# Optimization experiments

Measured on AMD Instinct MI355X. Metric: run time of the kernel, lower is better.

The kernel has to match this reference:

```python
import jax, jax.numpy as jnp
import numpy as np

MARGIN = 0.5
HIERARCHY_LEVEL = 0
EPS = 1e-05


def setup_inputs() -> dict:
    key = jax.random.key(0)
    k1, k2, k3, k4 = jax.random.split(key, 4)
    n, m, d, L, n_classes = 4096, 32768, 128, 2, 100
    embeddings = jax.random.normal(k1, (n, d), dtype=jnp.float32)
    ref_embeddings = jax.random.normal(k2, (m, d), dtype=jnp.float32)
    labels = jax.random.randint(k3, (n, L), 0, n_classes, dtype=jnp.int64)
    ref_labels = jax.random.randint(k4, (m, L), 0, n_classes, dtype=jnp.int64)
    return {"embeddings": embeddings, "labels": labels,
            "ref_embeddings": ref_embeddings, "ref_labels": ref_labels}


def reference(embeddings, labels, ref_embeddings, ref_labels):
    # select hierarchy level
    lab = labels[:, HIERARCHY_LEVEL]          # [n]
    ref_lab = ref_labels[:, HIERARCHY_LEVEL]  # [m]
    n = embeddings.shape[0]
    sim = embeddings @ ref_embeddings.T       # [n, m]
    same = lab[:, None] == ref_lab[None, :]   # [n, m] bool
    # positive pairs: same label and sim < 1 - eps -> contribute (1 - sim)
    pos_mask = same & (sim < 1.0 - EPS)
    # negative pairs: different label and sim > margin -> contribute sim
    neg_mask = (~same) & (sim > MARGIN)
    pos_loss = jnp.sum(jnp.where(pos_mask, 1.0 - sim, 0.0))
    neg_loss = jnp.sum(jnp.where(neg_mask, sim, 0.0))
    return (pos_loss + neg_loss) / n
```

## Files before the change

kernel.cpp:

```cpp
#include <hip/hip_runtime.h>
#include <stdint.h>

#define N_EMB 4096
#define M_REF 32768
#define D_K   128
#define NCLS  100
#define BM    128
#define BN    64
#define NT_PER 16
#define COLCHUNK (BN * NT_PER)
#define NCCHUNK (M_REF / COLCHUNK)
#define NROWT  (N_EMB / BM)
#define XBLOCKS (NROWT * NCCHUNK)
#define RCAP 192
#define CCAP 768

typedef __attribute__((ext_vector_type(8))) short short8;
typedef __attribute__((ext_vector_type(4))) float float4v;

static __device__ __forceinline__ unsigned short f2bf(float f) {
    unsigned int u = __builtin_bit_cast(unsigned int, f);
    u += 0x7FFFu + ((u >> 16) & 1u);
    return (unsigned short)(u >> 16);
}

#define CVT_THREADS (768 * 256)

__global__ void cvt_kernel(const float* __restrict__ emb, const float* __restrict__ ref,
                           unsigned short* __restrict__ aw, unsigned short* __restrict__ bw,
                           float* __restrict__ out) {
    const int NA4 = N_EMB * D_K / 4;
    int i0 = blockIdx.x * 256 + threadIdx.x;
    if (i0 == 0) *out = 0.0f;
    #pragma unroll
    for (int k = 0; k < 6; ++k) {
        int i = i0 + k * CVT_THREADS;
        const float4* src;
        unsigned short* dst;
        int j;
        if (i < NA4) { src = (const float4*)emb; dst = aw; j = i; }
        else         { src = (const float4*)ref; dst = bw; j = i - NA4; }
        float4 v = src[j];
        ushort4 o;
        o.x = f2bf(v.x); o.y = f2bf(v.y); o.z = f2bf(v.z); o.w = f2bf(v.w);
        *(ushort4*)(dst + (size_t)j * 4) = o;
    }
}

static __device__ __forceinline__ void gld_lds16(const void* g, void* l) {
    __builtin_amdgcn_global_load_lds((__attribute__((address_space(1))) void*)g,
                                     (__attribute__((address_space(3))) void*)l,
                                     16, 0, 0);
}

template<int NI>
static __device__ __forceinline__ void stage_rows(const unsigned short* __restrict__ g,
                                                  unsigned short* l, int tid) {
    const int rlow = tid >> 4;
    const int sc   = (tid & 15) ^ rlow;
    const char* g0 = (const char*)g + (rlow * D_K + sc * 8) * 2;
    char* l0 = (char*)l + tid * 16;
    #pragma unroll
    for (int i = 0; i < NI; ++i)
        gld_lds16(g0 + (size_t)i * (16 * D_K * 2), l0 + i * 4096);
}

static __device__ __forceinline__ void stage_gather(const unsigned short* __restrict__ base,
                                                    const int* idxlist, int count,
                                                    unsigned short* l, int tid) {
    const int rlow = tid >> 4;
    const int sc   = (tid & 15) ^ rlow;
    char* l0 = (char*)l + tid * 16;
    #pragma unroll
    for (int i = 0; i < 4; ++i) {
        int r = i * 16 + rlow;
        if (r < count) {
            int gi = idxlist[r];
            gld_lds16((const char*)base + ((size_t)gi * D_K + sc * 8) * 2, l0 + i * 4096);
        }
    }
}

__launch_bounds__(256, 4)
__global__ void xbm_kernel(const unsigned short* __restrict__ aw,
                           const unsigned short* __restrict__ bw,
                           const int* __restrict__ lab,
                           const int* __restrict__ rlab,
                           float* __restrict__ out) {
    __shared__ unsigned short b_sm[2][BN * D_K];
    __shared__ float red_sm[4];
    __shared__ int rlist[RCAP], clist[CCAP];
    __shared__ int rcnt_s, ccnt_s;

    const int tid  = threadIdx.x;
    const int lane = tid & 63;
    const int wave = tid >> 6;
    const int quad = lane >> 4;
    const int l15  = lane & 15;

    float bsum = 0.0f;

    if (blockIdx.x >= NCLS) {
        const int gid = blockIdx.x - NCLS;
        const int rtile  = gid >> 5;
        const int cchunk = gid & 31;
        const int row0 = rtile * BM;
        const int col0 = cchunk * COLCHUNK;

        stage_rows<8>(aw + (size_t)row0 * D_K, &b_sm[0][0], tid);
        __syncthreads();

        short8 a_reg[2][4];
        #pragma unroll
        for (int mt = 0; mt < 2; ++mt) {
            int ml = wave * 32 + mt * 16 + l15;
            #pragma unroll
            for (int ks = 0; ks < 4; ++ks) {
                int cs = (ks * 4 + quad) ^ l15;
                a_reg[mt][ks] = *(const short8*)(&b_sm[0][0] + (size_t)ml * D_K + cs * 8);
            }
        }
        __syncthreads();

        stage_rows<4>(bw + (size_t)col0 * D_K, b_sm[0], tid);

        float lsum[4] = {0.0f, 0.0f, 0.0f, 0.0f};

        #define COMPUTE_TILE(BP)                                                  \
            {                                                                     \
                const unsigned short* bp_ = (BP);                                 \
                float4v acc[2][4] = {};                                           \
                _Pragma("unroll")                                                 \
                for (int ks = 0; ks < 4; ++ks) {                                  \
                    short8 breg[4];                                               \
                    _Pragma("unroll")                                             \
                    for (int nt = 0; nt < 4; ++nt) {                              \
                        int nl = nt * 16 + l15;                                   \
                        int cs = (ks * 4 + quad) ^ l15;                           \
                        breg[nt] = *(const short8*)(bp_ + (size_t)nl * D_K + cs * 8); \
                    }                                                             \
                    _Pragma("unroll")                                             \
                    for (int mt = 0; mt < 2; ++mt)                                \
                        _Pragma("unroll")                                         \
                        for (int nt = 0; nt < 4; ++nt)                            \
                            acc[mt][nt] = __builtin_amdgcn_mfma_f32_16x16x32_bf16(\
                                a_reg[mt][ks], breg[nt], acc[mt][nt], 0, 0, 0);   \
                }                                                                 \
                _Pragma("unroll")                                                 \
                for (int mt = 0; mt < 2; ++mt)                                    \
                    _Pragma("unroll")                                             \
                    for (int nt = 0; nt < 4; ++nt)                                \
                        _Pragma("unroll")                                         \
                        for (int r = 0; r < 4; ++r) {                             \
                            float s = acc[mt][nt][r];                             \
                            lsum[r] += (s > 0.5f) ? s : 0.0f;                     \
                        }                                                         \
            }

        #pragma unroll 1
        for (int t = 0; t < NT_PER; t += 2) {
            __syncthreads();
            stage_rows<4>(bw + (size_t)(col0 + (t + 1) * BN) * D_K, b_sm[1], tid);
            COMPUTE_TILE(b_sm[0]);
            __syncthreads();
            if (t + 2 < NT_PER)
                stage_rows<4>(bw + (size_t)(col0 + (t + 2) * BN) * D_K, b_sm[0], tid);
            COMPUTE_TILE(b_sm[1]);
        }
        bsum = (lsum[0] + lsum[1]) + (lsum[2] + lsum[3]);
    } else {
        const int cls = blockIdx.x;

        if (tid == 0) { rcnt_s = 0; ccnt_s = 0; }
        __syncthreads();
        for (int i = tid; i < N_EMB; i += 256)
            if (lab[i * 2] == cls) {
                int p = atomicAdd(&rcnt_s, 1);
                if (p < RCAP) rlist[p] = i;
            }
        for (int j = tid; j < M_REF; j += 256)
            if (rlab[j * 2] == cls) {
                int p = atomicAdd(&ccnt_s, 1);
                if (p < CCAP) clist[p] = j;
            }
        __syncthreads();
        const int rn = min(rcnt_s, RCAP), cn = min(ccnt_s, CCAP);

        for (int r0 = 0; r0 < rn; r0 += 64) {
            const int rch = min(64, rn - r0);
            __syncthreads();
            stage_gather(aw, rlist + r0, rch, b_sm[0], tid);
            for (int c0 = 0; c0 < cn; c0 += 64) {
                const int cch = min(64, cn - c0);
                __syncthreads();
                stage_gather(bw, clist + c0, cch, b_sm[1], tid);
                __syncthreads();
                const int slot = wave * 16 + l15;
                const bool cvalid = slot < cch;
                #pragma unroll 1
                for (int mt = 0; mt < 4; ++mt) {
                    if (mt * 16 >= rch) break;
                    float4v acc = {0.0f, 0.0f, 0.0f, 0.0f};
                    #pragma unroll
                    for (int ks = 0; ks < 4; ++ks) {
                        int cs = (ks * 4 + quad) ^ l15;
                        short8 a = *(const short8*)(b_sm[0] + (size_t)(mt * 16 + l15) * D_K + cs * 8);
                        short8 b = *(const short8*)(b_sm[1] + (size_t)slot * D_K + cs * 8);
                        acc = __builtin_amdgcn_mfma_f32_16x16x32_bf16(a, b, acc, 0, 0, 0);
                    }
                    #pragma unroll
                    for (int r = 0; r < 4; ++r) {
                        int m_loc = mt * 16 + quad * 4 + r;
                        if (cvalid && m_loc < rch) {
                            float s = acc[r];
                            bsum += fmaxf(1.0f - s, 0.0f) - ((s > 0.5f) ? s : 0.0f);
                        }
                    }
                }
            }
        }
    }

    #pragma unroll
    for (int off = 32; off > 0; off >>= 1)
        bsum += __shfl_down(bsum, off, 64);
    if (lane == 0) red_sm[wave] = bsum;
    __syncthreads();
    if (tid == 0) {
        float v = (red_sm[0] + red_sm[1] + red_sm[2] + red_sm[3]) * (1.0f / (float)N_EMB);
        atomicAdd(out, v);
    }
}

extern "C" void kernel_launch(void* const* d_in, const int* in_sizes, int n_in,
                              void* d_out, int out_size, void* d_ws, size_t ws_size,
                              hipStream_t stream) {
    const float* emb     = (const float*)d_in[0];
    const int*   labels  = (const int*)d_in[1];
    const float* ref     = (const float*)d_in[2];
    const int*   rlabels = (const int*)d_in[3];
    float* out = (float*)d_out;

    unsigned short* aw = (unsigned short*)d_ws;
    unsigned short* bw = aw + (size_t)N_EMB * D_K;

    cvt_kernel<<<768, 256, 0, stream>>>(emb, ref, aw, bw, out);
    xbm_kernel<<<XBLOCKS + NCLS, 256, 0, stream>>>(aw, bw, labels, rlabels, out);
}
```

Baseline: 127.0 us.

## Widen GEMM tile to 128x128 and build class lists in the convert kernel

```diff
diff --git a/kernel.cpp b/kernel.cpp
--- a/kernel.cpp
+++ b/kernel.cpp
@@ -6,7 +6,7 @@
 #define D_K   128
 #define NCLS  100
 #define BM    128
-#define BN    64
+#define BN    128
 #define NT_PER 16
 #define COLCHUNK (BN * NT_PER)
 #define NCCHUNK (M_REF / COLCHUNK)
@@ -28,22 +28,41 @@
 
 __global__ void cvt_kernel(const float* __restrict__ emb, const float* __restrict__ ref,
                            unsigned short* __restrict__ aw, unsigned short* __restrict__ bw,
+                           const int* __restrict__ lab, const int* __restrict__ rlab,
+                           int* __restrict__ cnt_row, int* __restrict__ cnt_col,
+                           int* __restrict__ rowlist, int* __restrict__ collist,
                            float* __restrict__ out) {
-    const int NA4 = N_EMB * D_K / 4;
-    int i0 = blockIdx.x * 256 + threadIdx.x;
-    if (i0 == 0) *out = 0.0f;
-    #pragma unroll
-    for (int k = 0; k < 6; ++k) {
-        int i = i0 + k * CVT_THREADS;
-        const float4* src;
-        unsigned short* dst;
-        int j;
-        if (i < NA4) { src = (const float4*)emb; dst = aw; j = i; }
-        else         { src = (const float4*)ref; dst = bw; j = i - NA4; }
-        float4 v = src[j];
-        ushort4 o;
-        o.x = f2bf(v.x); o.y = f2bf(v.y); o.z = f2bf(v.z); o.w = f2bf(v.w);
-        *(ushort4*)(dst + (size_t)j * 4) = o;
+    if (blockIdx.x < 768) {
+        const int NA4 = N_EMB * D_K / 4;
+        int i0 = blockIdx.x * 256 + threadIdx.x;
+        if (i0 == 0) *out = 0.0f;
+        #pragma unroll
+        for (int k = 0; k < 6; ++k) {
+            int i = i0 + k * CVT_THREADS;
+            const float4* src;
+            unsigned short* dst;
+            int j;
+            if (i < NA4) { src = (const float4*)emb; dst = aw; j = i; }
+            else         { src = (const float4*)ref; dst = bw; j = i - NA4; }
+            float4 v = src[j];
+            ushort4 o;
+            o.x = f2bf(v.x); o.y = f2bf(v.y); o.z = f2bf(v.z); o.w = f2bf(v.w);
+            *(ushort4*)(dst + (size_t)j * 4) = o;
+        }
+    } else {
+        int t = (blockIdx.x - 768) * 256 + threadIdx.x;
+        {
+            int c = lab[t * 2];
+            int p = atomicAdd(&cnt_row[c], 1);
+            if (p < RCAP) rowlist[c * RCAP + p] = t;
+        }
+        #pragma unroll
+        for (int k = 0; k < 8; ++k) {
+            int j = t + k * 4096;
+            int c = rlab[j * 2];
+            int p = atomicAdd(&cnt_col[c], 1);
+            if (p < CCAP) collist[c * CCAP + p] = j;
+        }
     }
 }
 
@@ -66,7 +85,7 @@
 }
 
 static __device__ __forceinline__ void stage_gather(const unsigned short* __restrict__ base,
-                                                    const int* idxlist, int count,
+                                                    const int* __restrict__ idxlist, int count,
                                                     unsigned short* l, int tid) {
     const int rlow = tid >> 4;
     const int sc   = (tid & 15) ^ rlow;
@@ -81,16 +100,14 @@
     }
 }
 
-__launch_bounds__(256, 4)
+__launch_bounds__(256, 2)
 __global__ void xbm_kernel(const unsigned short* __restrict__ aw,
                            const unsigned short* __restrict__ bw,
-                           const int* __restrict__ lab,
-                           const int* __restrict__ rlab,
+                           const int* __restrict__ cnt_row, const int* __restrict__ cnt_col,
+                           const int* __restrict__ rowlist, const int* __restrict__ collist,
                            float* __restrict__ out) {
     __shared__ unsigned short b_sm[2][BN * D_K];
     __shared__ float red_sm[4];
-    __shared__ int rlist[RCAP], clist[CCAP];
-    __shared__ int rcnt_s, ccnt_s;
 
     const int tid  = threadIdx.x;
     const int lane = tid & 63;
@@ -102,18 +119,19 @@
 
     if (blockIdx.x >= NCLS) {
         const int gid = blockIdx.x - NCLS;
-        const int rtile  = gid >> 5;
-        const int cchunk = gid & 31;
+        const int rtile  = gid >> 4;
+        const int cchunk = gid & 15;
         const int row0 = rtile * BM;
         const int col0 = cchunk * COLCHUNK;
+        const int wm = wave >> 1, wn = wave & 1;
 
         stage_rows<8>(aw + (size_t)row0 * D_K, &b_sm[0][0], tid);
         __syncthreads();
 
-        short8 a_reg[2][4];
+        short8 a_reg[4][4];
         #pragma unroll
-        for (int mt = 0; mt < 2; ++mt) {
-            int ml = wave * 32 + mt * 16 + l15;
+        for (int mt = 0; mt < 4; ++mt) {
+            int ml = wm * 64 + mt * 16 + l15;
             #pragma unroll
             for (int ks = 0; ks < 4; ++ks) {
                 int cs = (ks * 4 + quad) ^ l15;
@@ -122,32 +140,32 @@
         }
         __syncthreads();
 
-        stage_rows<4>(bw + (size_t)col0 * D_K, b_sm[0], tid);
+        stage_rows<8>(bw + (size_t)col0 * D_K, b_sm[0], tid);
 
         float lsum[4] = {0.0f, 0.0f, 0.0f, 0.0f};
 
         #define COMPUTE_TILE(BP)                                                  \
             {                                                                     \
                 const unsigned short* bp_ = (BP);                                 \
-                float4v acc[2][4] = {};                                           \
+                float4v acc[4][4] = {};                                           \
                 _Pragma("unroll")                                                 \
                 for (int ks = 0; ks < 4; ++ks) {                                  \
                     short8 breg[4];                                               \
                     _Pragma("unroll")                                             \
                     for (int nt = 0; nt < 4; ++nt) {                              \
-                        int nl = nt * 16 + l15;                                   \
+                        int nl = wn * 64 + nt * 16 + l15;                         \
                         int cs = (ks * 4 + quad) ^ l15;                           \
                         breg[nt] = *(const short8*)(bp_ + (size_t)nl * D_K + cs * 8); \
                     }                                                             \
                     _Pragma("unroll")                                             \
-                    for (int mt = 0; mt < 2; ++mt)                                \
+                    for (int mt = 0; mt < 4; ++mt)                                \
                         _Pragma("unroll")                                         \
                         for (int nt = 0; nt < 4; ++nt)                            \
                             acc[mt][nt] = __builtin_amdgcn_mfma_f32_16x16x32_bf16(\
                                 a_reg[mt][ks], breg[nt], acc[mt][nt], 0, 0, 0);   \
                 }                                                                 \
                 _Pragma("unroll")                                                 \
-                for (int mt = 0; mt < 2; ++mt)                                    \
+                for (int mt = 0; mt < 4; ++mt)                                    \
                     _Pragma("unroll")                                             \
                     for (int nt = 0; nt < 4; ++nt)                                \
                         _Pragma("unroll")                                         \
@@ -160,31 +178,19 @@
         #pragma unroll 1
         for (int t = 0; t < NT_PER; t += 2) {
             __syncthreads();
-            stage_rows<4>(bw + (size_t)(col0 + (t + 1) * BN) * D_K, b_sm[1], tid);
+            stage_rows<8>(bw + (size_t)(col0 + (t + 1) * BN) * D_K, b_sm[1], tid);
             COMPUTE_TILE(b_sm[0]);
             __syncthreads();
             if (t + 2 < NT_PER)
-                stage_rows<4>(bw + (size_t)(col0 + (t + 2) * BN) * D_K, b_sm[0], tid);
+                stage_rows<8>(bw + (size_t)(col0 + (t + 2) * BN) * D_K, b_sm[0], tid);
             COMPUTE_TILE(b_sm[1]);
         }
         bsum = (lsum[0] + lsum[1]) + (lsum[2] + lsum[3]);
     } else {
         const int cls = blockIdx.x;
-
-        if (tid == 0) { rcnt_s = 0; ccnt_s = 0; }
-        __syncthreads();
-        for (int i = tid; i < N_EMB; i += 256)
-            if (lab[i * 2] == cls) {
-                int p = atomicAdd(&rcnt_s, 1);
-                if (p < RCAP) rlist[p] = i;
-            }
-        for (int j = tid; j < M_REF; j += 256)
-            if (rlab[j * 2] == cls) {
-                int p = atomicAdd(&ccnt_s, 1);
-                if (p < CCAP) clist[p] = j;
-            }
-        __syncthreads();
-        const int rn = min(rcnt_s, RCAP), cn = min(ccnt_s, CCAP);
+        const int rn = min(cnt_row[cls], RCAP), cn = min(cnt_col[cls], CCAP);
+        const int* rlist = rowlist + cls * RCAP;
+        const int* clist = collist + cls * CCAP;
 
         for (int r0 = 0; r0 < rn; r0 += 64) {
             const int rch = min(64, rn - r0);
@@ -241,9 +247,18 @@
     const int*   rlabels = (const int*)d_in[3];
     float* out = (float*)d_out;
 
-    unsigned short* aw = (unsigned short*)d_ws;
-    unsigned short* bw = aw + (size_t)N_EMB * D_K;
-
-    cvt_kernel<<<768, 256, 0, stream>>>(emb, ref, aw, bw, out);
-    xbm_kernel<<<XBLOCKS + NCLS, 256, 0, stream>>>(aw, bw, labels, rlabels, out);
-}
+    char* ws = (char*)d_ws;
+    unsigned short* aw = (unsigned short*)ws;
+    unsigned short* bw = (unsigned short*)(ws + 0x100000);
+    int* cnt_row  = (int*)(ws + 0x900000);
+    int* cnt_col  = (int*)(ws + 0x900200);
+    int* rowlist  = (int*)(ws + 0x900400);
+    int* collist  = (int*)(ws + 0x913400);
+
+    hipMemsetAsync(ws + 0x900000, 0, 0x400, stream);
+    cvt_kernel<<<784, 256, 0, stream>>>(emb, ref, aw, bw,
+                                        (const int*)labels, (const int*)rlabels,
+                                        cnt_row, cnt_col, rowlist, collist, out);
+    xbm_kernel<<<XBLOCKS + NCLS, 256, 0, stream>>>(aw, bw,
+                                                   cnt_row, cnt_col, rowlist, collist, out);
+}
```

Result: slower. 148.6 us (+17.0%).

## Fuse label comparison into dense GEMM epilogue, drop per-class gather blocks

Applied to the files above, without the earlier changes.

```diff
diff --git a/kernel.cpp b/kernel.cpp
--- a/kernel.cpp
+++ b/kernel.cpp
@@ -4,7 +4,6 @@
 #define N_EMB 4096
 #define M_REF 32768
 #define D_K   128
-#define NCLS  100
 #define BM    128
 #define BN    64
 #define NT_PER 16
@@ -12,8 +11,6 @@
 #define NCCHUNK (M_REF / COLCHUNK)
 #define NROWT  (N_EMB / BM)
 #define XBLOCKS (NROWT * NCCHUNK)
-#define RCAP 192
-#define CCAP 768
 
 typedef __attribute__((ext_vector_type(8))) short short8;
 typedef __attribute__((ext_vector_type(4))) float float4v;
@@ -65,23 +62,7 @@
         gld_lds16(g0 + (size_t)i * (16 * D_K * 2), l0 + i * 4096);
 }
 
-static __device__ __forceinline__ void stage_gather(const unsigned short* __restrict__ base,
-                                                    const int* idxlist, int count,
-                                                    unsigned short* l, int tid) {
-    const int rlow = tid >> 4;
-    const int sc   = (tid & 15) ^ rlow;
-    char* l0 = (char*)l + tid * 16;
-    #pragma unroll
-    for (int i = 0; i < 4; ++i) {
-        int r = i * 16 + rlow;
-        if (r < count) {
-            int gi = idxlist[r];
-            gld_lds16((const char*)base + ((size_t)gi * D_K + sc * 8) * 2, l0 + i * 4096);
-        }
-    }
-}
-
-__launch_bounds__(256, 4)
+__launch_bounds__(256, 3)
 __global__ void xbm_kernel(const unsigned short* __restrict__ aw,
                            const unsigned short* __restrict__ bw,
                            const int* __restrict__ lab,
@@ -89,8 +70,6 @@
                            float* __restrict__ out) {
     __shared__ unsigned short b_sm[2][BN * D_K];
     __shared__ float red_sm[4];
-    __shared__ int rlist[RCAP], clist[CCAP];
-    __shared__ int rcnt_s, ccnt_s;
 
     const int tid  = threadIdx.x;
     const int lane = tid & 63;
@@ -98,133 +77,93 @@
     const int quad = lane >> 4;
     const int l15  = lane & 15;
 
-    float bsum = 0.0f;
+    const int rtile  = blockIdx.x >> 5;
+    const int cchunk = blockIdx.x & 31;
+    const int row0 = rtile * BM;
+    const int col0 = cchunk * COLCHUNK;
 
-    if (blockIdx.x >= NCLS) {
-        const int gid = blockIdx.x - NCLS;
-        const int rtile  = gid >> 5;
-        const int cchunk = gid & 31;
-        const int row0 = rtile * BM;
-        const int col0 = cchunk * COLCHUNK;
+    stage_rows<8>(aw + (size_t)row0 * D_K, &b_sm[0][0], tid);
 
-        stage_rows<8>(aw + (size_t)row0 * D_K, &b_sm[0][0], tid);
-        __syncthreads();
+    int labv[2][4];
+    #pragma unroll
+    for (int mt = 0; mt < 2; ++mt)
+        #pragma unroll
+        for (int r = 0; r < 4; ++r)
+            labv[mt][r] = lab[(row0 + wave * 32 + mt * 16 + quad * 4 + r) * 2];
 
-        short8 a_reg[2][4];
+    __syncthreads();
+
+    short8 a_reg[2][4];
+    #pragma unroll
+    for (int mt = 0; mt < 2; ++mt) {
+        int ml = wave * 32 + mt * 16 + l15;
         #pragma unroll
-        for (int mt = 0; mt < 2; ++mt) {
-            int ml = wave * 32 + mt * 16 + l15;
-            #pragma unroll
-            for (int ks = 0; ks < 4; ++ks) {
-                int cs = (ks * 4 + quad) ^ l15;
-                a_reg[mt][ks] = *(const short8*)(&b_sm[0][0] + (size_t)ml * D_K + cs * 8);
-            }
+        for (int ks = 0; ks < 4; ++ks) {
+            int cs = (ks * 4 + quad) ^ l15;
+            a_reg[mt][ks] = *(const short8*)(&b_sm[0][0] + (size_t)ml * D_K + cs * 8);
         }
-        __syncthreads();
+    }
+    __syncthreads();
 
-        stage_rows<4>(bw + (size_t)col0 * D_K, b_sm[0], tid);
+    stage_rows<4>(bw + (size_t)col0 * D_K, b_sm[0], tid);
 
-        float lsum[4] = {0.0f, 0.0f, 0.0f, 0.0f};
+    float lsum[4] = {0.0f, 0.0f, 0.0f, 0.0f};
 
-        #define COMPUTE_TILE(BP)                                                  \
-            {                                                                     \
-                const unsigned short* bp_ = (BP);                                 \
-                float4v acc[2][4] = {};                                           \
+    #define COMPUTE_TILE(BP, CBASE)                                               \
+        {                                                                         \
+            const unsigned short* bp_ = (BP);                                     \
+            const int cb_ = (CBASE);                                              \
+            int rl[4];                                                            \
+            _Pragma("unroll")                                                     \
+            for (int nt = 0; nt < 4; ++nt)                                        \
+                rl[nt] = rlab[(cb_ + nt * 16 + l15) * 2];                         \
+            float4v acc[2][4] = {};                                               \
+            _Pragma("unroll")                                                     \
+            for (int ks = 0; ks < 4; ++ks) {                                      \
+                short8 breg[4];                                                   \
                 _Pragma("unroll")                                                 \
-                for (int ks = 0; ks < 4; ++ks) {                                  \
-                    short8 breg[4];                                               \
-                    _Pragma("unroll")                                             \
-                    for (int nt = 0; nt < 4; ++nt) {                              \
-                        int nl = nt * 16 + l15;                                   \
-                        int cs = (ks * 4 + quad) ^ l15;                           \
-                        breg[nt] = *(const short8*)(bp_ + (size_t)nl * D_K + cs * 8); \
-                    }                                                             \
-                    _Pragma("unroll")                                             \
-                    for (int mt = 0; mt < 2; ++mt)                                \
-                        _Pragma("unroll")                                         \
-                        for (int nt = 0; nt < 4; ++nt)                            \
-                            acc[mt][nt] = __builtin_amdgcn_mfma_f32_16x16x32_bf16(\
-                                a_reg[mt][ks], breg[nt], acc[mt][nt], 0, 0, 0);   \
+                for (int nt = 0; nt < 4; ++nt) {                                  \
+                    int nl = nt * 16 + l15;                                       \
+                    int cs = (ks * 4 + quad) ^ l15;                               \
+                    breg[nt] = *(const short8*)(bp_ + (size_t)nl * D_K + cs * 8); \
                 }                                                                 \
                 _Pragma("unroll")                                                 \
                 for (int mt = 0; mt < 2; ++mt)                                    \
                     _Pragma("unroll")                                             \
                     for (int nt = 0; nt < 4; ++nt)                                \
-                        _Pragma("unroll")                                         \
-                        for (int r = 0; r < 4; ++r) {                             \
-                            float s = acc[mt][nt][r];                             \
-                            lsum[r] += (s > 0.5f) ? s : 0.0f;                     \
-                        }                                                         \
-            }
+                        acc[mt][nt] = __builtin_amdgcn_mfma_f32_16x16x32_bf16(    \
+                            a_reg[mt][ks], breg[nt], acc[mt][nt], 0, 0, 0);       \
+            }                                                                     \
+            _Pragma("unroll")                                                     \
+            for (int mt = 0; mt < 2; ++mt)                                        \
+                _Pragma("unroll")                                                 \
+                for (int nt = 0; nt < 4; ++nt)                                    \
+                    _Pragma("unroll")                                             \
+                    for (int r = 0; r < 4; ++r) {                                 \
+                        float s = acc[mt][nt][r];                                 \
+                               \
+                        float pos = fmaxf(1.0f - s, 0.0f);                        \
+                        float neg = (s > 0.5f) ? s : 0.0f;                        \
+                        lsum[r] += (labv[mt][r] == rl[nt]) ? pos : neg;           \
+                    }                                                             \
+        }
 
-        #pragma unroll 1
-        for (int t = 0; t < NT_PER; t += 2) {
-            __syncthreads();
-            stage_rows<4>(bw + (size_t)(col0 + (t + 1) * BN) * D_K, b_sm[1], tid);
-            COMPUTE_TILE(b_sm[0]);
-            __syncthreads();
-            if (t + 2 < NT_PER)
-                stage_rows<4>(bw + (size_t)(col0 + (t + 2) * BN) * D_K, b_sm[0], tid);
-            COMPUTE_TILE(b_sm[1]);
-        }
-        bsum = (lsum[0] + lsum[1]) + (lsum[2] + lsum[3]);
-    } else {
-        const int cls = blockIdx.x;
-
-        if (tid == 0) { rcnt_s = 0; ccnt_s = 0; }
+    #pragma unroll 1
+    for (int t = 0; t < NT_PER; t += 2) {
         __syncthreads();
-        for (int i = tid; i < N_EMB; i += 256)
-            if (lab[i * 2] == cls) {
-                int p = atomicAdd(&rcnt_s, 1);
-                if (p < RCAP) rlist[p] = i;
-            }
-        for (int j = tid; j < M_REF; j += 256)
-            if (rlab[j * 2] == cls) {
-                int p = atomicAdd(&ccnt_s, 1);
-                if (p < CCAP) clist[p] = j;
-            }
+        stage_rows<4>(bw + (size_t)(col0 + (t + 1) * BN) * D_K, b_sm[1], tid);
+        COMPUTE_TILE(b_sm[0], col0 + t * BN);
         __syncthreads();
-        const int rn = min(rcnt_s, RCAP), cn = min(ccnt_s, CCAP);
-
-        for (int r0 = 0; r0 < rn; r0 += 64) {
-            const int rch = min(64, rn - r0);
-            __syncthreads();
-            stage_gather(aw, rlist + r0, rch, b_sm[0], tid);
-            for (int c0 = 0; c0 < cn; c0 += 64) {
-                const int cch = min(64, cn - c0);
-                __syncthreads();
-                stage_gather(bw, clist + c0, cch, b_sm[1], tid);
-                __syncthreads();
-                const int slot = wave * 16 + l15;
-                const bool cvalid = slot < cch;
-                #pragma unroll 1
-                for (int mt = 0; mt < 4; ++mt) {
-                    if (mt * 16 >= rch) break;
-                    float4v acc = {0.0f, 0.0f, 0.0f, 0.0f};
-                    #pragma unroll
-                    for (int ks = 0; ks < 4; ++ks) {
-                        int cs = (ks * 4 + quad) ^ l15;
-                        short8 a = *(const short8*)(b_sm[0] + (size_t)(mt * 16 + l15) * D_K + cs * 8);
-                        short8 b = *(const short8*)(b_sm[1] + (size_t)slot * D_K + cs * 8);
-                        acc = __builtin_amdgcn_mfma_f32_16x16x32_bf16(a, b, acc, 0, 0, 0);
-                    }
-                    #pragma unroll
-                    for (int r = 0; r < 4; ++r) {
-                        int m_loc = mt * 16 + quad * 4 + r;
-                        if (cvalid && m_loc < rch) {
-                            float s = acc[r];
-                            bsum += fmaxf(1.0f - s, 0.0f) - ((s > 0.5f) ? s : 0.0f);
-                        }
-                    }
-                }
-            }
-        }
+        if (t + 2 < NT_PER)
+            stage_rows<4>(bw + (size_t)(col0 + (t + 2) * BN) * D_K, b_sm[0], tid);
+        COMPUTE_TILE(b_sm[1], col0 + (t + 1) * BN);
     }
 
+    float loss = (lsum[0] + lsum[1]) + (lsum[2] + lsum[3]);
     #pragma unroll
     for (int off = 32; off > 0; off >>= 1)
-        bsum += __shfl_down(bsum, off, 64);
-    if (lane == 0) red_sm[wave] = bsum;
+        loss += __shfl_down(loss, off, 64);
+    if (lane == 0) red_sm[wave] = loss;
     __syncthreads();
     if (tid == 0) {
         float v = (red_sm[0] + red_sm[1] + red_sm[2] + red_sm[3]) * (1.0f / (float)N_EMB);
@@ -245,5 +184,6 @@
     unsigned short* bw = aw + (size_t)N_EMB * D_K;
 
     cvt_kernel<<<768, 256, 0, stream>>>(emb, ref, aw, bw, out);
-    xbm_kernel<<<XBLOCKS + NCLS, 256, 0, stream>>>(aw, bw, labels, rlabels, out);
+    xbm_kernel<<<XBLOCKS, 256, 0, stream>>>(aw, bw,
+                                            (const int*)labels, (const int*)rlabels, out);
 }
```

Result: faster. 120.3 us (-5.2%).
